# Optimization experiments

Measured on AMD Instinct MI355X. Metric: run time of the kernel, lower is better.

The kernel has to match this reference:

```python
import jax, jax.numpy as jnp
import numpy as np

NEG_INF = 100000.0  # matches torch INF tensor in source


def setup_inputs() -> dict:
    key = jax.random.key(0)
    ks = jax.random.split(key, 8)
    B, S, D = 4, 4096, 256
    query = jax.random.normal(ks[0], (B, S, D), dtype=jnp.float32)
    k_in = jax.random.normal(ks[1], (B, S, D), dtype=jnp.float32)
    value = jax.random.normal(ks[2], (B, S, D), dtype=jnp.float32)
    mask = jax.random.randint(ks[3], (B, S), 0, 2).astype(bool)
    # nn.Linear(dim, dim) params: weight [out, in], bias [out]
    lim = 1.0 / np.sqrt(D)
    Wq = jax.random.uniform(ks[4], (D, D), jnp.float32, -lim, lim)
    bq = jax.random.uniform(ks[5], (D,), jnp.float32, -lim, lim)
    Wk = jax.random.uniform(ks[6], (D, D), jnp.float32, -lim, lim)
    bk = jax.random.uniform(ks[7], (D,), jnp.float32, -lim, lim)
    return {"query": query, "key": k_in, "value": value, "mask": mask,
            "Wq": Wq, "bq": bq, "Wk": Wk, "bk": bk}


def reference(query, key, value, mask, Wq, bq, Wk, bk):
    D = query.shape[-1]
    q = jnp.einsum('bsd,ed->bse', query, Wq) + bq  # query_proj
    k = jnp.einsum('bsd,ed->bse', key, Wk) + bk    # key_proj
    score = jnp.einsum('bqd,bkd->bqk', q, k) / jnp.sqrt(jnp.float32(D))
    # mask (B,S) broadcast over last dim: masks whole query rows where mask is False
    score = jnp.where(mask[:, :, None], score, -NEG_INF)
    attn = jax.nn.softmax(score, axis=-1)  # [B, S, S]
    context = jnp.einsum('bqk,bkd->bqd', attn, value)
    return (context, attn)
```

## Files before the change

### kernel.cpp

```cpp
#include <hip/hip_runtime.h>

typedef __attribute__((ext_vector_type(8))) _Float16 f16x8;
typedef __attribute__((ext_vector_type(4))) _Float16 f16x4;
typedef __attribute__((ext_vector_type(4))) float f32x4;
typedef _Float16 half_t;

#define MFMA32(a, b, c) __builtin_amdgcn_mfma_f32_16x16x32_f16((a), (b), (c), 0, 0, 0)
#define MFMA16(a, b, c) __builtin_amdgcn_mfma_f32_16x16x16f16((a), (b), (c), 0, 0, 0)

__device__ __forceinline__ void gload_lds16(const half_t* g, half_t* l) {
    __builtin_amdgcn_global_load_lds(
        (const __attribute__((address_space(1))) unsigned int*)g,
        (__attribute__((address_space(3))) unsigned int*)l, 16, 0, 0);
}


__global__ __launch_bounds__(512, 2)
void proj_kernel(const float* __restrict__ X, const float* __restrict__ W,
                 const float* __restrict__ bias, half_t* __restrict__ out)
{
    __shared__ half_t Wl[256 * 264];
    int tid = threadIdx.x;
    for (int i = 0; i < 128; ++i) {
        int idx = tid + i * 512;
        int r = idx >> 8, c = idx & 255;
        Wl[r * 264 + c] = (half_t)W[idx];
    }
    __syncthreads();

    int w = tid >> 6, lane = tid & 63, l15 = lane & 15, hi = lane >> 4;
    int row0 = blockIdx.x * 128 + w * 16;

    const float* xb = X + (size_t)(row0 + l15) * 256 + hi * 8;
    f32x4 acc[16];
#pragma unroll
    for (int n = 0; n < 16; ++n) acc[n] = (f32x4){0.f, 0.f, 0.f, 0.f};

#pragma unroll
    for (int kd = 0; kd < 8; ++kd) {
        const float4* xv = (const float4*)(xb + kd * 32);
        float4 x0 = xv[0], x1 = xv[1];
        f16x8 a = { (half_t)x0.x, (half_t)x0.y, (half_t)x0.z, (half_t)x0.w,
                    (half_t)x1.x, (half_t)x1.y, (half_t)x1.z, (half_t)x1.w };
#pragma unroll
        for (int n = 0; n < 16; ++n) {
            f16x8 bf = *(const f16x8*)&Wl[(n * 16 + l15) * 264 + kd * 32 + hi * 8];
            acc[n] = MFMA32(a, bf, acc[n]);
        }
    }

#pragma unroll
    for (int n = 0; n < 16; ++n) {
        float bv = bias[n * 16 + l15];
#pragma unroll
        for (int r = 0; r < 4; ++r) {
            float v = acc[n][r] + bv;
            out[(size_t)(row0 + 4 * hi + r) * 256 + n * 16 + l15] = (half_t)v;
        }
    }
}

__global__ __launch_bounds__(256)
void vt_kernel(const float* __restrict__ V, half_t* __restrict__ vt)
{
    __shared__ half_t tile[64][65];
    int tid = threadIdx.x;
    int b = blockIdx.x >> 8, rest = blockIdx.x & 255;
    int s0 = (rest >> 2) * 64, d0 = (rest & 3) * 64;
#pragma unroll
    for (int i = 0; i < 16; ++i) {
        int srow = i * 4 + (tid >> 6);
        int dcol = tid & 63;
        tile[srow][dcol] = (half_t)V[(size_t)(b * 4096 + s0 + srow) * 256 + d0 + dcol];
    }
    __syncthreads();
#pragma unroll
    for (int i = 0; i < 16; ++i) {
        int drow = i * 4 + (tid >> 6);
        int scol = tid & 63;
        vt[(size_t)(b * 256 + d0 + drow) * 4096 + s0 + scol] = tile[scol][drow];
    }
}

__global__ __launch_bounds__(512, 2)
void attn_kernel(const half_t* __restrict__ qh, const half_t* __restrict__ kg_,
                 const half_t* __restrict__ vt, const int* __restrict__ mask,
                 float* __restrict__ ctx_out, float* __restrict__ attn_out)
{
    __shared__ __align__(16) char pool[131072 + 1024];
    half_t* Klds = (half_t*)pool;
    half_t* Vlds = (half_t*)(pool + 65536);
    float*  redsum = (float*)(pool + 131072);

    const int tid = threadIdx.x;
    const int w = tid >> 6, lane = tid & 63, l15 = lane & 15, hi = lane >> 4;
    const int qg = w >> 2, khs = w & 3;
    const int bid = blockIdx.x;
    const int wgid = (bid & 7) * 32 + (bid >> 3);
    const int b = wgid >> 6, q0 = (wgid & 63) * 64;

    const half_t* kg = kg_ + (size_t)b * 4096 * 256;
    const half_t* vg = vt + (size_t)b * 256 * 4096;

    bool km[2];
    f16x8 qf[2][8];
#pragma unroll
    for (int qs = 0; qs < 2; ++qs) {
        int q = q0 + qg * 32 + qs * 16 + l15;
        km[qs] = mask[b * 4096 + q] != 0;
        const half_t* qb = qh + (size_t)(b * 4096 + q) * 256 + hi * 8;
#pragma unroll
        for (int kd = 0; kd < 8; ++kd) qf[qs][kd] = *(const f16x8*)(qb + kd * 32);
    }

    auto stageK = [&](int t, int buf) {
#pragma unroll
        for (int i = 0; i < 4; ++i) {
            int row = w * 8 + i * 2 + (lane >> 5);
            int u = lane & 31;
            const half_t* src = kg + (size_t)(t * 64 + row) * 256 + (u ^ (row & 7)) * 8;
            gload_lds16(src, Klds + buf * 16384 + (w * 8 + i * 2) * 256);
        }
    };
    auto stageV = [&](int t, int buf) {
#pragma unroll
        for (int i = 0; i < 4; ++i) {
            int d = w * 32 + i * 8 + (lane >> 3);
            int u = lane & 7;
            const half_t* src = vg + (size_t)d * 4096 + t * 64 + (u ^ (d & 7)) * 8;
            gload_lds16(src, Vlds + buf * 16384 + (w * 32 + i * 8) * 64);
        }
    };

    const int arow = khs * 16 + l15;
    const int asw = arow & 7;

    stageK(0, 0);
    __syncthreads();
    float vsum0 = 0.f, vsum1 = 0.f;
    for (int t = 0; t < 64; ++t) {
        if (t < 63) stageK(t + 1, (t + 1) & 1);
        const half_t* ab = Klds + (t & 1) * 16384 + arow * 256;
        f32x4 c0 = {0.f,0.f,0.f,0.f}, c1 = {0.f,0.f,0.f,0.f};
#pragma unroll
        for (int kd = 0; kd < 8; ++kd) {
            f16x8 A = *(const f16x8*)(ab + ((kd * 4 + hi) ^ asw) * 8);
            c0 = MFMA32(A, qf[0][kd], c0);
            c1 = MFMA32(A, qf[1][kd], c1);
        }
#pragma unroll
        for (int r = 0; r < 4; ++r) {
            vsum0 += __expf(km[0] ? c0[r] * 0.0625f : 0.0f);
            vsum1 += __expf(km[1] ? c1[r] * 0.0625f : 0.0f);
        }
        __syncthreads();
    }
    vsum0 += __shfl_xor(vsum0, 16, 64);
    vsum0 += __shfl_xor(vsum0, 32, 64);
    vsum1 += __shfl_xor(vsum1, 16, 64);
    vsum1 += __shfl_xor(vsum1, 32, 64);
    if (lane < 16) {
        redsum[((qg * 4 + khs) * 2 + 0) * 16 + l15] = vsum0;
        redsum[((qg * 4 + khs) * 2 + 1) * 16 + l15] = vsum1;
    }
    __syncthreads();
    float inv0 = 0.f, inv1 = 0.f;
    {
        float s0 = 0.f, s1 = 0.f;
#pragma unroll
        for (int k = 0; k < 4; ++k) {
            s0 += redsum[((qg * 4 + k) * 2 + 0) * 16 + l15];
            s1 += redsum[((qg * 4 + k) * 2 + 1) * 16 + l15];
        }
        inv0 = 1.0f / s0;
        inv1 = 1.0f / s1;
    }

    f32x4 acc[2][16];
#pragma unroll
    for (int qs = 0; qs < 2; ++qs)
#pragma unroll
        for (int n = 0; n < 16; ++n) acc[qs][n] = (f32x4){0.f, 0.f, 0.f, 0.f};

    stageK(0, 0); stageV(0, 0);
    __syncthreads();

    float* aout0 = attn_out + (size_t)(b * 4096 + q0 + qg * 32 + l15) * 4096 + khs * 16 + 4 * hi;
    float* aout1 = aout0 + (size_t)16 * 4096;

    for (int t = 0; t < 64; ++t) {
        if (t < 63) { stageK(t + 1, (t + 1) & 1); stageV(t + 1, (t + 1) & 1); }

        const half_t* ab = Klds + (t & 1) * 16384 + arow * 256;
        f32x4 c0 = {0.f,0.f,0.f,0.f}, c1 = {0.f,0.f,0.f,0.f};
#pragma unroll
        for (int kd = 0; kd < 8; ++kd) {
            f16x8 A = *(const f16x8*)(ab + ((kd * 4 + hi) ^ asw) * 8);
            c0 = MFMA32(A, qf[0][kd], c0);
            c1 = MFMA32(A, qf[1][kd], c1);
        }
        f32x4 a0, a1;
#pragma unroll
        for (int r = 0; r < 4; ++r) {
            a0[r] = __expf(km[0] ? c0[r] * 0.0625f : 0.0f) * inv0;
            a1[r] = __expf(km[1] ? c1[r] * 0.0625f : 0.0f) * inv1;
        }
        *(f32x4*)(aout0 + t * 64) = a0;
        *(f32x4*)(aout1 + t * 64) = a1;

        f16x4 p0 = { (half_t)a0[0], (half_t)a0[1], (half_t)a0[2], (half_t)a0[3] };
        f16x4 p1 = { (half_t)a1[0], (half_t)a1[1], (half_t)a1[2], (half_t)a1[3] };

        const half_t* vb = Vlds + (t & 1) * 16384;
#pragma unroll
        for (int n = 0; n < 16; ++n) {
            int d = n * 16 + l15;
            f16x4 Bv = *(const f16x4*)(vb + d * 64 + (((khs * 32 + hi * 8) ^ ((d & 7) << 4)) >> 1));
            acc[0][n] = MFMA16(p0, Bv, acc[0][n]);
            acc[1][n] = MFMA16(p1, Bv, acc[1][n]);
        }
        __syncthreads();
    }

    float* rc = (float*)pool + qg * (32 * 256);
    for (int rnd = 0; rnd < 4; ++rnd) {
        if (khs == rnd) {
#pragma unroll
            for (int qs = 0; qs < 2; ++qs)
#pragma unroll
                for (int n = 0; n < 16; ++n)
#pragma unroll
                    for (int r = 0; r < 4; ++r) {
                        int idx = (qs * 16 + 4 * hi + r) * 256 + n * 16 + l15;
                        if (rnd == 0) rc[idx] = acc[qs][n][r];
                        else          rc[idx] += acc[qs][n][r];
                    }
        }
        __syncthreads();
    }

    float* cbase = ctx_out + (size_t)(b * 4096 + q0) * 256;
    for (int e = tid * 4; e < 64 * 256; e += 512 * 4)
        *(f32x4*)(cbase + e) = *(const f32x4*)((const float*)pool + e);
}

extern "C" void kernel_launch(void* const* d_in, const int* in_sizes, int n_in,
                              void* d_out, int out_size, void* d_ws, size_t ws_size,
                              hipStream_t stream) {
    const float* query = (const float*)d_in[0];
    const float* key   = (const float*)d_in[1];
    const float* value = (const float*)d_in[2];
    const int*   mask  = (const int*)d_in[3];
    const float* Wq    = (const float*)d_in[4];
    const float* bq    = (const float*)d_in[5];
    const float* Wk    = (const float*)d_in[6];
    const float* bk    = (const float*)d_in[7];

    float* ctx  = (float*)d_out;
    float* attn = ctx + (size_t)4 * 4096 * 256;

    half_t* qh = (half_t*)d_ws;
    half_t* kh = qh + (size_t)4 * 4096 * 256;
    half_t* vt = kh + (size_t)4 * 4096 * 256;

    proj_kernel<<<128, 512, 0, stream>>>(query, Wq, bq, qh);
    proj_kernel<<<128, 512, 0, stream>>>(key,   Wk, bk, kh);
    vt_kernel<<<1024, 256, 0, stream>>>(value, vt);
    attn_kernel<<<256, 512, 0, stream>>>(qh, kh, vt, mask, ctx, attn);
}
```

Before: 235.2 us.

## Double attention workgroup to 1024 threads with one 16-row query slice per wave

The attention kernel now launches 1024 threads per workgroup (16 waves) instead of 512. Each wave handles one 16-row query slice instead of two, which halves the per-wave accumulator and Q-fragment registers and spreads K/V staging across more waves. The probability-matrix stores become nontemporal so the large attention output does not pollute cache. The tradeoffs are more waves synchronising at each barrier, the same 129KB LDS per workgroup, and the launch_bounds(1024,4) occupancy hint, which may not be achievable given that LDS footprint.

Result: slower. 247.8 us (+5.4%).

```diff
diff --git a/kernel.cpp b/kernel.cpp
--- a/kernel.cpp
+++ b/kernel.cpp
@@ -82,7 +82,7 @@
     }
 }
 
-__global__ __launch_bounds__(512, 2)
+__global__ __launch_bounds__(1024, 4)
 void attn_kernel(const half_t* __restrict__ qh, const half_t* __restrict__ kg_,
                  const half_t* __restrict__ vt, const int* __restrict__ mask,
                  float* __restrict__ ctx_out, float* __restrict__ attn_out)
@@ -98,37 +98,34 @@
     const int bid = blockIdx.x;
     const int wgid = (bid & 7) * 32 + (bid >> 3);
     const int b = wgid >> 6, q0 = (wgid & 63) * 64;
+    const int q = q0 + qg * 16 + l15;
 
     const half_t* kg = kg_ + (size_t)b * 4096 * 256;
     const half_t* vg = vt + (size_t)b * 256 * 4096;
 
-    bool km[2];
-    f16x8 qf[2][8];
-#pragma unroll
-    for (int qs = 0; qs < 2; ++qs) {
-        int q = q0 + qg * 32 + qs * 16 + l15;
-        km[qs] = mask[b * 4096 + q] != 0;
-        const half_t* qb = qh + (size_t)(b * 4096 + q) * 256 + hi * 8;
-#pragma unroll
-        for (int kd = 0; kd < 8; ++kd) qf[qs][kd] = *(const f16x8*)(qb + kd * 32);
-    }
+    const bool km = mask[b * 4096 + q] != 0;
+
+    f16x8 qf[8];
+    const half_t* qb = qh + (size_t)(b * 4096 + q) * 256 + hi * 8;
+#pragma unroll
+    for (int kd = 0; kd < 8; ++kd) qf[kd] = *(const f16x8*)(qb + kd * 32);
 
     auto stageK = [&](int t, int buf) {
 #pragma unroll
-        for (int i = 0; i < 4; ++i) {
-            int row = w * 8 + i * 2 + (lane >> 5);
+        for (int i = 0; i < 2; ++i) {
+            int row = w * 4 + i * 2 + (lane >> 5);
             int u = lane & 31;
             const half_t* src = kg + (size_t)(t * 64 + row) * 256 + (u ^ (row & 7)) * 8;
-            gload_lds16(src, Klds + buf * 16384 + (w * 8 + i * 2) * 256);
+            gload_lds16(src, Klds + buf * 16384 + (w * 4 + i * 2) * 256);
         }
     };
     auto stageV = [&](int t, int buf) {
 #pragma unroll
-        for (int i = 0; i < 4; ++i) {
-            int d = w * 32 + i * 8 + (lane >> 3);
+        for (int i = 0; i < 2; ++i) {
+            int d = w * 16 + i * 8 + (lane >> 3);
             int u = lane & 7;
             const half_t* src = vg + (size_t)d * 4096 + t * 64 + (u ^ (d & 7)) * 8;
-            gload_lds16(src, Vlds + buf * 16384 + (w * 32 + i * 8) * 64);
+            gload_lds16(src, Vlds + buf * 16384 + (w * 16 + i * 8) * 64);
         }
     };
 
@@ -137,110 +134,84 @@
 
     stageK(0, 0);
     __syncthreads();
-    float vsum0 = 0.f, vsum1 = 0.f;
+    float vsum = 0.f;
     for (int t = 0; t < 64; ++t) {
         if (t < 63) stageK(t + 1, (t + 1) & 1);
         const half_t* ab = Klds + (t & 1) * 16384 + arow * 256;
-        f32x4 c0 = {0.f,0.f,0.f,0.f}, c1 = {0.f,0.f,0.f,0.f};
+        f32x4 c = {0.f, 0.f, 0.f, 0.f};
 #pragma unroll
         for (int kd = 0; kd < 8; ++kd) {
             f16x8 A = *(const f16x8*)(ab + ((kd * 4 + hi) ^ asw) * 8);
-            c0 = MFMA32(A, qf[0][kd], c0);
-            c1 = MFMA32(A, qf[1][kd], c1);
-        }
-#pragma unroll
-        for (int r = 0; r < 4; ++r) {
-            vsum0 += __expf(km[0] ? c0[r] * 0.0625f : 0.0f);
-            vsum1 += __expf(km[1] ? c1[r] * 0.0625f : 0.0f);
-        }
+            c = MFMA32(A, qf[kd], c);
+        }
+#pragma unroll
+        for (int r = 0; r < 4; ++r)
+            vsum += __expf(km ? c[r] * 0.0625f : 0.0f);
         __syncthreads();
     }
-    vsum0 += __shfl_xor(vsum0, 16, 64);
-    vsum0 += __shfl_xor(vsum0, 32, 64);
-    vsum1 += __shfl_xor(vsum1, 16, 64);
-    vsum1 += __shfl_xor(vsum1, 32, 64);
-    if (lane < 16) {
-        redsum[((qg * 4 + khs) * 2 + 0) * 16 + l15] = vsum0;
-        redsum[((qg * 4 + khs) * 2 + 1) * 16 + l15] = vsum1;
-    }
-    __syncthreads();
-    float inv0 = 0.f, inv1 = 0.f;
-    {
-        float s0 = 0.f, s1 = 0.f;
-#pragma unroll
-        for (int k = 0; k < 4; ++k) {
-            s0 += redsum[((qg * 4 + k) * 2 + 0) * 16 + l15];
-            s1 += redsum[((qg * 4 + k) * 2 + 1) * 16 + l15];
-        }
-        inv0 = 1.0f / s0;
-        inv1 = 1.0f / s1;
-    }
-
-    f32x4 acc[2][16];
-#pragma unroll
-    for (int qs = 0; qs < 2; ++qs)
-#pragma unroll
-        for (int n = 0; n < 16; ++n) acc[qs][n] = (f32x4){0.f, 0.f, 0.f, 0.f};
+    vsum += __shfl_xor(vsum, 16, 64);
+    vsum += __shfl_xor(vsum, 32, 64);
+    if (lane < 16) redsum[(qg * 4 + khs) * 16 + l15] = vsum;
+    __syncthreads();
+    const float inv = 1.0f / (redsum[(qg * 4 + 0) * 16 + l15] +
+                              redsum[(qg * 4 + 1) * 16 + l15] +
+                              redsum[(qg * 4 + 2) * 16 + l15] +
+                              redsum[(qg * 4 + 3) * 16 + l15]);
+
+    f32x4 acc[16];
+#pragma unroll
+    for (int n = 0; n < 16; ++n) acc[n] = (f32x4){0.f, 0.f, 0.f, 0.f};
 
     stageK(0, 0); stageV(0, 0);
     __syncthreads();
 
-    float* aout0 = attn_out + (size_t)(b * 4096 + q0 + qg * 32 + l15) * 4096 + khs * 16 + 4 * hi;
-    float* aout1 = aout0 + (size_t)16 * 4096;
+    float* aout = attn_out + (size_t)(b * 4096 + q) * 4096 + khs * 16 + 4 * hi;
 
     for (int t = 0; t < 64; ++t) {
         if (t < 63) { stageK(t + 1, (t + 1) & 1); stageV(t + 1, (t + 1) & 1); }
 
         const half_t* ab = Klds + (t & 1) * 16384 + arow * 256;
-        f32x4 c0 = {0.f,0.f,0.f,0.f}, c1 = {0.f,0.f,0.f,0.f};
+        f32x4 c = {0.f, 0.f, 0.f, 0.f};
 #pragma unroll
         for (int kd = 0; kd < 8; ++kd) {
             f16x8 A = *(const f16x8*)(ab + ((kd * 4 + hi) ^ asw) * 8);
-            c0 = MFMA32(A, qf[0][kd], c0);
-            c1 = MFMA32(A, qf[1][kd], c1);
-        }
-        f32x4 a0, a1;
-#pragma unroll
-        for (int r = 0; r < 4; ++r) {
-            a0[r] = __expf(km[0] ? c0[r] * 0.0625f : 0.0f) * inv0;
-            a1[r] = __expf(km[1] ? c1[r] * 0.0625f : 0.0f) * inv1;
-        }
-        *(f32x4*)(aout0 + t * 64) = a0;
-        *(f32x4*)(aout1 + t * 64) = a1;
-
-        f16x4 p0 = { (half_t)a0[0], (half_t)a0[1], (half_t)a0[2], (half_t)a0[3] };
-        f16x4 p1 = { (half_t)a1[0], (half_t)a1[1], (half_t)a1[2], (half_t)a1[3] };
+            c = MFMA32(A, qf[kd], c);
+        }
+        f32x4 a;
+#pragma unroll
+        for (int r = 0; r < 4; ++r)
+            a[r] = __expf(km ? c[r] * 0.0625f : 0.0f) * inv;
+        __builtin_nontemporal_store(a, (f32x4*)(aout + t * 64));
+
+        f16x4 p = { (half_t)a[0], (half_t)a[1], (half_t)a[2], (half_t)a[3] };
 
         const half_t* vb = Vlds + (t & 1) * 16384;
 #pragma unroll
         for (int n = 0; n < 16; ++n) {
             int d = n * 16 + l15;
             f16x4 Bv = *(const f16x4*)(vb + d * 64 + (((khs * 32 + hi * 8) ^ ((d & 7) << 4)) >> 1));
-            acc[0][n] = MFMA16(p0, Bv, acc[0][n]);
-            acc[1][n] = MFMA16(p1, Bv, acc[1][n]);
+            acc[n] = MFMA16(p, Bv, acc[n]);
         }
         __syncthreads();
     }
 
-    float* rc = (float*)pool + qg * (32 * 256);
+    float* rc = (float*)pool + qg * (16 * 256);
     for (int rnd = 0; rnd < 4; ++rnd) {
         if (khs == rnd) {
 #pragma unroll
-            for (int qs = 0; qs < 2; ++qs)
-#pragma unroll
-                for (int n = 0; n < 16; ++n)
-#pragma unroll
-                    for (int r = 0; r < 4; ++r) {
-                        int idx = (qs * 16 + 4 * hi + r) * 256 + n * 16 + l15;
-                        if (rnd == 0) rc[idx] = acc[qs][n][r];
-                        else          rc[idx] += acc[qs][n][r];
-                    }
+            for (int n = 0; n < 16; ++n)
+#pragma unroll
+                for (int r = 0; r < 4; ++r) {
+                    int idx = (4 * hi + r) * 256 + n * 16 + l15;
+                    if (rnd == 0) rc[idx] = acc[n][r];
+                    else          rc[idx] += acc[n][r];
+                }
         }
         __syncthreads();
     }
 
     float* cbase = ctx_out + (size_t)(b * 4096 + q0) * 256;
-    for (int e = tid * 4; e < 64 * 256; e += 512 * 4)
+    for (int e = tid * 4; e < 64 * 256; e += 1024 * 4)
         *(f32x4*)(cbase + e) = *(const f32x4*)((const float*)pool + e);
 }
 
@@ -266,5 +237,5 @@
     proj_kernel<<<128, 512, 0, stream>>>(query, Wq, bq, qh);
     proj_kernel<<<128, 512, 0, stream>>>(key,   Wk, bk, kh);
     vt_kernel<<<1024, 256, 0, stream>>>(value, vt);
-    attn_kernel<<<256, 512, 0, stream>>>(qh, kh, vt, mask, ctx, attn);
-}
+    attn_kernel<<<256, 1024, 0, stream>>>(qh, kh, vt, mask, ctx, attn);
+}
```
